# Kernel optimization log

Hardware: AMD Instinct MI355X
Metric: run time of the kernel (lower is better)

## Reference

```python
import jax, jax.numpy as jnp
import numpy as np

B, H, W = 8, 512, 512
N_INST = 8
N_SIGMA = 2
FG_W = 1.0
W_INST, W_VAR, W_SEED = 1.0, 10.0, 1.0


def make_yxm():
    xm = jnp.broadcast_to(jnp.linspace(0.0, 1.0, W)[None, None, :], (1, H, W))
    ym = jnp.broadcast_to(jnp.linspace(0.0, 1.0, H)[None, :, None], (1, H, W))
    return jnp.concatenate([ym, xm], 0)  # [2,H,W]


def lovasz_hinge(logits, labels):
    # logits, labels: [P]; labels in {0,1}
    signs = 2.0 * labels - 1.0
    errors = 1.0 - logits * signs
    order = jnp.argsort(-errors)
    errors_s = errors[order]
    gt_s = labels[order]
    gts = gt_s.sum()
    intersection = gts - jnp.cumsum(gt_s)
    union = gts + jnp.cumsum(1.0 - gt_s)
    jac = 1.0 - intersection / union
    jac = jnp.concatenate([jac[:1], jac[1:] - jac[:-1]])
    return jnp.dot(jax.nn.relu(errors_s), jax.lax.stop_gradient(jac))


def seg_item(pred, inst, label, center_img, yxm):
    spatial_emb = jnp.tanh(pred[0:2]) + yxm            # [2,H,W]
    sigma = jax.nn.sigmoid(pred[2:2 + N_SIGMA])        # [2,H,W]
    seed = jax.nn.sigmoid(pred[2 + N_SIGMA])           # [H,W]
    seed_loss = jnp.sum(jnp.where(label == 0, seed * seed, 0.0))

    def per_inst(iid):
        in_mask = (inst == iid)
        cmask = in_mask & center_img
        valid = (cmask.sum() == 1)                      # exactly one center pixel
        m = in_mask.astype(pred.dtype)
        npix = jnp.maximum(m.sum(), 1.0)
        center = jnp.sum(yxm * cmask, axis=(1, 2))      # [2]
        s_mean = jnp.sum(sigma * m, axis=(1, 2)) / npix # [2]
        var_l = jnp.sum(((sigma - jax.lax.stop_gradient(s_mean)[:, None, None]) ** 2) * m) / (N_SIGMA * npix)
        s = jnp.exp(s_mean * 10.0)
        dist = jnp.exp(-jnp.sum(((spatial_emb - center[:, None, None]) ** 2) * s[:, None, None], axis=0))
        inst_l = lovasz_hinge((dist * 2.0 - 1.0).ravel(), m.ravel())
        seed_l = jnp.sum(((seed - jax.lax.stop_gradient(dist)) ** 2) * m)
        v = valid.astype(pred.dtype)
        return inst_l * v, var_l * v, seed_l * v

    il, vl, sl = jax.vmap(per_inst)(jnp.arange(1, N_INST + 1))
    # NOTE: source never increments obj_count in the seg loop, so no division.
    seed_total = (seed_loss + FG_W * sl.sum()) / (H * W)
    return W_INST * il.sum() + W_VAR * vl.sum() + W_SEED * seed_total


def tra_item(pred, inst, center_img, offset, yxm):
    emb = yxm - jnp.tanh(pred[0:2])
    sigma = jax.nn.sigmoid(pred[2:2 + N_SIGMA])

    def per_inst(iid):
        in_mask = (inst == iid)
        cmask = in_mask & center_img
        center = jnp.sum(yxm * cmask, axis=(1, 2))          # [2]
        off_c = jnp.sum(offset * cmask, axis=(1, 2))        # [2]
        gt_c = center - off_c / 256.0
        valid = (cmask.sum() == 1) & (gt_c.min() >= 0.0) & (gt_c.max() <= 1.0)
        m = in_mask.astype(pred.dtype)
        npix = jnp.maximum(m.sum(), 1.0)
        s_mean = jnp.sum(sigma * m, axis=(1, 2)) / npix
        var_l = jnp.sum(((sigma - jax.lax.stop_gradient(s_mean)[:, None, None]) ** 2) * m)  # sum (not mean)
        s = jnp.exp(s_mean * 10.0)
        dist = jnp.exp(-jnp.sum(((emb - gt_c[:, None, None]) ** 2) * s[:, None, None], axis=0))
        tl = lovasz_hinge((dist * 2.0 - 1.0).ravel(), m.ravel())
        v = valid.astype(pred.dtype)
        return tl * v, var_l * v, v

    tl, vl, vs = jax.vmap(per_inst)(jnp.arange(1, N_INST + 1))
    cnt = jnp.maximum(vs.sum(), 1.0)
    return W_INST * (tl.sum() / cnt) + W_VAR * (vl.sum() / cnt)


def setup_inputs() -> dict:
    key = jax.random.key(0)
    k1, k2, k3 = jax.random.split(key, 3)
    inst = np.zeros((H, W), np.int32)
    cen = np.zeros((H, W), bool)
    for i in range(N_INST):
        ty, tx = i // 2, i % 2
        cy, cx = ty * 128 + 64, tx * 256 + 128
        inst[cy - 40:cy + 40, cx - 40:cx + 40] = i + 1
        cen[cy, cx] = True
    instances = jnp.tile(jnp.asarray(inst)[None], (B, 1, 1))
    center_images = jnp.tile(jnp.asarray(cen)[None], (B, 1, 1))
    labels = (instances > 0).astype(jnp.int32)
    return {
        "segmentation_predictions": jax.random.normal(k1, (B, 3 + N_SIGMA, H, W), jnp.float32),
        "tracking_predictions": jax.random.normal(k2, (B // 2, 2 + N_SIGMA, H, W), jnp.float32),
        "instances": instances,
        "labels": labels,
        "center_images": center_images,
        "offsets": jax.random.normal(k3, (B // 2, 2, H, W), jnp.float32),
    }


def reference(segmentation_predictions, tracking_predictions, instances, labels, center_images, offsets):
    yxm = make_yxm()
    seg = jax.vmap(seg_item, in_axes=(0, 0, 0, 0, None))(
        segmentation_predictions, instances, labels, center_images, yxm)
    half = B // 2
    tra = jax.vmap(tra_item, in_axes=(0, 0, 0, 0, None))(
        tracking_predictions, instances[:half], center_images[:half], offsets, yxm)
    return seg.sum() + tra.sum()
```

## Files before the change

kernel.cpp:

```cpp
#include <hip/hip_runtime.h>
#include <cstdint>
#include <cstddef>

#define HW (512 * 512)
#define NB3 512
#define NPAIR 96
#define THRQ 6.3f
#define BSCALE 256.0f

__device__ __forceinline__ float sigmoidf_(float x) {
    return 1.0f / (1.0f + __expf(-x));
}
__device__ __forceinline__ float tanhf_(float x) {
    float e = __expf(2.0f * x);
    return 1.0f - 2.0f / (e + 1.0f);
}
__device__ __forceinline__ float wred(float v) {
#pragma unroll
    for (int o = 32; o > 0; o >>= 1) v += __shfl_down(v, o, 64);
    return v;
}
__device__ __forceinline__ unsigned wredu(unsigned v) {
#pragma unroll
    for (int o = 32; o > 0; o >>= 1) v += __shfl_down(v, o, 64);
    return v;
}

__global__ __launch_bounds__(256) void zero_ws_k(unsigned* ws, int n) {
    int i = blockIdx.x * 256 + threadIdx.x;
    if (i < n) ws[i] = 0u;
}

__global__ __launch_bounds__(256) void reduce_k(
    const float* __restrict__ segp, const float* __restrict__ trap,
    const int* __restrict__ inst, const int* __restrict__ cen,
    const float* __restrict__ off,
    float* __restrict__ pacc, float* __restrict__ seedloss)
{
    __shared__ float part[4][41];
    int item = blockIdx.y;
    bool isseg = item < 8;
    int ii = isseg ? item : item - 8;
    const float* pb = isseg ? segp + (size_t)item * 5 * HW
                            : trap + (size_t)ii * 4 * HW;
    const int* ib = inst + (size_t)ii * HW;
    const int* cb = cen + (size_t)ii * HW;
    const float* ob = off + (size_t)ii * 2 * HW;
    int pairBase = (isseg ? 0 : 64) + ii * 8;

    float npx[8], a0[8], q0[8], a1[8], q1[8];
#pragma unroll
    for (int j = 0; j < 8; j++) { npx[j]=0.f; a0[j]=0.f; q0[j]=0.f; a1[j]=0.f; q1[j]=0.f; }
    float sacc = 0.f;

    int base = blockIdx.x * 4096;
    for (int it = 0; it < 4; ++it) {
        int idx = base + (it * 256 + threadIdx.x) * 4;
        int4 v4 = *(const int4*)&ib[idx];
        const int vs[4] = { v4.x, v4.y, v4.z, v4.w };
        if (isseg) {
            float4 x4 = *(const float4*)&pb[4 * HW + idx];
            const float ss[4] = { x4.x, x4.y, x4.z, x4.w };
#pragma unroll
            for (int c = 0; c < 4; c++) {
                if (vs[c] == 0) { float sd = sigmoidf_(ss[c]); sacc += sd * sd; }
            }
        }
        if ((v4.x | v4.y | v4.z | v4.w) != 0) {
            float4 x2 = *(const float4*)&pb[2 * HW + idx];
            float4 x3 = *(const float4*)&pb[3 * HW + idx];
            int4 c4 = *(const int4*)&cb[idx];
            const float s2s[4] = { x2.x, x2.y, x2.z, x2.w };
            const float s3s[4] = { x3.x, x3.y, x3.z, x3.w };
            const int cs[4] = { c4.x, c4.y, c4.z, c4.w };
#pragma unroll
            for (int c = 0; c < 4; c++) {
                int v = vs[c];
                if (v == 0) continue;
                float s0 = sigmoidf_(s2s[c]);
                float s1 = sigmoidf_(s3s[c]);
                float s00 = s0 * s0, s11 = s1 * s1;
#pragma unroll
                for (int j = 0; j < 8; j++) {
                    float f = (v == j + 1) ? 1.0f : 0.0f;
                    npx[j] += f;
                    a0[j] += f * s0; q0[j] += f * s00;
                    a1[j] += f * s1; q1[j] += f * s11;
                }
                if (cs[c] != 0 && v >= 1 && v <= 8) {
                    int idxc = idx + c;
                    int pair = pairBase + (v - 1);
                    int y = idxc >> 9, x = idxc & 511;
                    atomicAdd(&pacc[pair * 10 + 5], (float)y * (1.0f / 511.0f));
                    atomicAdd(&pacc[pair * 10 + 6], (float)x * (1.0f / 511.0f));
                    atomicAdd(&pacc[pair * 10 + 7], 1.0f);
                    if (!isseg) {
                        atomicAdd(&pacc[pair * 10 + 8], ob[idxc]);
                        atomicAdd(&pacc[pair * 10 + 9], ob[HW + idxc]);
                    }
                }
            }
        }
    }
    int lane = threadIdx.x & 63, wave = threadIdx.x >> 6;
#pragma unroll
    for (int j = 0; j < 8; j++) {
        float r0 = wred(npx[j]), r1 = wred(a0[j]), r2 = wred(q0[j]);
        float r3 = wred(a1[j]), r4 = wred(q1[j]);
        if (lane == 0) {
            part[wave][j * 5 + 0] = r0; part[wave][j * 5 + 1] = r1;
            part[wave][j * 5 + 2] = r2; part[wave][j * 5 + 3] = r3;
            part[wave][j * 5 + 4] = r4;
        }
    }
    {
        float rs = wred(sacc);
        if (lane == 0) part[wave][40] = rs;
    }
    __syncthreads();
    int t = threadIdx.x;
    if (t < 41) {
        float s = part[0][t] + part[1][t] + part[2][t] + part[3][t];
        if (t < 40) {
            int pair = pairBase + t / 5, comp = t % 5;
            atomicAdd(&pacc[pair * 10 + comp], s);
        } else if (isseg) {
            atomicAdd(&seedloss[item], s);
        }
    }
}

__global__ __launch_bounds__(256) void hist_k(
    const float* __restrict__ segp, const float* __restrict__ trap,
    const int* __restrict__ inst, const float* __restrict__ pacc,
    unsigned* __restrict__ hneg, unsigned* __restrict__ hpos,
    float* __restrict__ seedl)
{
    __shared__ unsigned hh[8 * NB3 + 8];
    __shared__ float prm[8][4];
    int item = blockIdx.y;
    bool isseg = item < 8;
    int ii = isseg ? item : item - 8;
    int tid = threadIdx.x;
    int pairBase = (isseg ? 0 : 64) + ii * 8;

    for (int i = tid; i < 8 * NB3 + 8; i += 256) hh[i] = 0u;
    if (tid < 8) {
        const float* a = pacc + (size_t)(pairBase + tid) * 10;
        float np = fmaxf(a[0], 1.0f);
        float cy = a[5], cx = a[6];
        if (!isseg) { cy -= a[8] * (1.0f / 256.0f); cx -= a[9] * (1.0f / 256.0f); }
        prm[tid][0] = cy;
        prm[tid][1] = cx;
        prm[tid][2] = __expf(10.0f * a[1] / np);
        prm[tid][3] = __expf(10.0f * a[3] / np);
    }
    __syncthreads();

    float cyR[8], cxR[8], s0R[8], s1R[8];
#pragma unroll
    for (int j = 0; j < 8; j++) {
        cyR[j] = prm[j][0]; cxR[j] = prm[j][1];
        s0R[j] = prm[j][2]; s1R[j] = prm[j][3];
    }
    const float* pb = isseg ? segp + (size_t)item * 5 * HW
                            : trap + (size_t)ii * 4 * HW;
    const int* ib = inst + (size_t)ii * HW;

    unsigned cnt0[8];
#pragma unroll
    for (int j = 0; j < 8; j++) cnt0[j] = 0u;

    int base = blockIdx.x * 2048;
    for (int it = 0; it < 4; ++it) {
        int idx = base + (it * 256 + tid) * 2;
        int2 v2 = *(const int2*)&ib[idx];
        float2 f0 = *(const float2*)&pb[idx];
        float2 f1 = *(const float2*)&pb[HW + idx];
        const int vv[2] = { v2.x, v2.y };
        const float p0s[2] = { f0.x, f0.y };
        const float p1s[2] = { f1.x, f1.y };
#pragma unroll
        for (int c = 0; c < 2; c++) {
            int idxc = idx + c;
            int v = vv[c];
            int y = idxc >> 9, x = idxc & 511;
            float ym = (float)y * (1.0f / 511.0f);
            float xm = (float)x * (1.0f / 511.0f);
            float t0 = tanhf_(p0s[c]), t1 = tanhf_(p1s[c]);
            float e0 = isseg ? (t0 + ym) : (ym - t0);
            float e1 = isseg ? (t1 + xm) : (xm - t1);
            unsigned sbits = 0u;
#pragma unroll
            for (int j = 0; j < 8; j++) {
                float d0 = e0 - cyR[j], d1 = e1 - cxR[j];
                float q = fmaf(d0 * d0, s0R[j], d1 * d1 * s1R[j]);
                bool m = (v == j + 1);
                bool slow = m || (q <= THRQ);
                sbits |= (slow ? 1u : 0u) << j;
                cnt0[j] += slow ? 0u : 1u;
            }
            while (sbits) {
                int j = __ffs(sbits) - 1;
                sbits &= sbits - 1u;
                float d0 = e0 - prm[j][0], d1 = e1 - prm[j][1];
                float q = fmaf(d0 * d0, prm[j][2], d1 * d1 * prm[j][3]);
                float dd = __expf(-q);
                bool m = (v == j + 1);
                float e = m ? fmaf(-2.0f, dd, 2.0f) : 2.0f * dd;
                int bin = (int)(e * BSCALE);
                if (bin > NB3 - 1) bin = NB3 - 1;
                atomicAdd(&hh[j * NB3 + bin], m ? 0x10000u : 1u);
                if (m && isseg) {
                    float sd = sigmoidf_(pb[4 * HW + idxc]);
                    float df = sd - dd;
                    atomicAdd((float*)&hh[8 * NB3 + j], df * df);
                }
            }
        }
    }
    int lane = tid & 63;
#pragma unroll
    for (int j = 0; j < 8; j++) {
        unsigned r = wredu(cnt0[j]);
        if (lane == 0 && r) atomicAdd(&hh[j * NB3], r);
    }
    __syncthreads();

#pragma unroll
    for (int j = 0; j < 8; j++) {
        size_t gb = (size_t)(pairBase + j) * NB3;
        for (int i = tid; i < NB3; i += 256) {
            unsigned hv = hh[j * NB3 + i];
            if (hv) {
                unsigned n = hv & 0xFFFFu, p = hv >> 16;
                if (n) atomicAdd(&hneg[gb + i], n);
                if (p) atomicAdd(&hpos[gb + i], p);
            }
        }
    }
    if (isseg && tid < 8) {
        float sv = __uint_as_float(hh[8 * NB3 + tid]);
        if (sv != 0.0f) atomicAdd(&seedl[pairBase + tid], sv);
    }
}

__global__ __launch_bounds__(64) void scan_k(
    const unsigned* __restrict__ hneg, const unsigned* __restrict__ hpos,
    float* __restrict__ lov)
{
    int pair = blockIdx.x;
    int lane = threadIdx.x;
    const unsigned* hn = hneg + (size_t)pair * NB3;
    const unsigned* hp = hpos + (size_t)pair * NB3;

    unsigned hnv[8], hpv[8];
    float ck = 0.f, cp = 0.f;
#pragma unroll
    for (int i = 0; i < 8; i++) {
        int bn = NB3 - 1 - (lane * 8 + i);
        unsigned a = hn[bn], b = hp[bn];
        hnv[i] = a; hpv[i] = b;
        ck += (float)(a + b); cp += (float)b;
    }
    float ik = ck, ip = cp;
#pragma unroll
    for (int o = 1; o < 64; o <<= 1) {
        float nk = __shfl_up(ik, o, 64), np2 = __shfl_up(ip, o, 64);
        if (lane >= o) { ik += nk; ip += np2; }
    }
    float P = __shfl(ip, 63, 64);
    float k = ik - ck;
    float p = ip - cp;
    float acc = 0.f;
#pragma unroll
    for (int i = 0; i < 8; i++) {
        float cn = (float)hnv[i], cpp = (float)hpv[i];
        float c = cn + cpp;
        if (c > 0.f) {
            float Jb = (k > 0.f) ? (1.0f - (P - p) / (P + k - p)) : 0.0f;
            k += c; p += cpp;
            float Ja = 1.0f - (P - p) / (P + k - p);
            int bn = NB3 - 1 - (lane * 8 + i);
            acc += ((float)bn + 0.5f) * (2.0f / NB3) * (Ja - Jb);
        }
    }
    acc = wred(acc);
    if (lane == 0) lov[pair] = acc;
}

__global__ __launch_bounds__(128) void combine_k(
    const float* __restrict__ pacc, const float* __restrict__ lov,
    const float* __restrict__ seedl, const float* __restrict__ seedloss,
    float* __restrict__ out)
{
    __shared__ float svalid[NPAIR], svar[NPAIR];
    int t = threadIdx.x;
    if (t < NPAIR) {
        const float* a = pacc + (size_t)t * 10;
        float npraw = a[0];
        float np = fmaxf(npraw, 1.0f);
        float v0 = fmaxf(a[2] - a[1] * a[1] / np, 0.0f);
        float v1 = fmaxf(a[4] - a[3] * a[3] / np, 0.0f);
        float cc = a[7];
        float valid, varl;
        if (t < 64) {
            varl = (v0 + v1) / (2.0f * np);
            valid = (cc > 0.5f && cc < 1.5f) ? 1.0f : 0.0f;
        } else {
            varl = v0 + v1;
            float gy = a[5] - a[8] * (1.0f / 256.0f);
            float gx = a[6] - a[9] * (1.0f / 256.0f);
            valid = (cc > 0.5f && cc < 1.5f &&
                     gy >= 0.0f && gy <= 1.0f && gx >= 0.0f && gx <= 1.0f) ? 1.0f : 0.0f;
        }
        svalid[t] = valid; svar[t] = varl;
    }
    __syncthreads();
    if (t == 0) {
        double total = 0.0;
        for (int b = 0; b < 8; b++) {
            double s = 0.0, sl = 0.0;
            for (int j = 0; j < 8; j++) {
                int pr = b * 8 + j;
                double v = svalid[pr];
                s += v * ((double)lov[pr] + 10.0 * (double)svar[pr]);
                sl += v * (double)seedl[pr];
            }
            total += s + ((double)seedloss[b] + sl) / (double)HW;
        }
        for (int tt = 0; tt < 4; tt++) {
            double tl = 0.0, vl = 0.0, cnt = 0.0;
            for (int j = 0; j < 8; j++) {
                int pr = 64 + tt * 8 + j;
                double v = svalid[pr];
                tl += v * (double)lov[pr];
                vl += v * (double)svar[pr];
                cnt += v;
            }
            if (cnt < 1.0) cnt = 1.0;
            total += tl / cnt + 10.0 * vl / cnt;
        }
        *out = (float)total;
    }
}

extern "C" void kernel_launch(void* const* d_in, const int* in_sizes, int n_in,
                              void* d_out, int out_size, void* d_ws, size_t ws_size,
                              hipStream_t stream)
{
    const float* segp = (const float*)d_in[0];
    const float* trap = (const float*)d_in[1];
    const int* inst   = (const int*)d_in[2];
    const int* cen    = (const int*)d_in[4];
    const float* off  = (const float*)d_in[5];
    float* out = (float*)d_out;

    unsigned* hneg = (unsigned*)d_ws;
    unsigned* hpos = hneg + (size_t)NPAIR * NB3;
    float* pacc = (float*)(hpos + (size_t)NPAIR * NB3);
    float* seedloss = pacc + NPAIR * 10;
    float* seedl = seedloss + 8;
    float* lov = seedl + NPAIR;
    size_t total_words = (size_t)NPAIR * NB3 * 2 + NPAIR * 10 + 8 + NPAIR + NPAIR;

    zero_ws_k<<<(int)((total_words + 255) / 256), 256, 0, stream>>>((unsigned*)d_ws, (int)total_words);
    reduce_k<<<dim3(64, 12), 256, 0, stream>>>(segp, trap, inst, cen, off, pacc, seedloss);
    hist_k<<<dim3(128, 12), 256, 0, stream>>>(segp, trap, inst, pacc, hneg, hpos, seedl);
    scan_k<<<NPAIR, 64, 0, stream>>>(hneg, hpos, lov);
    combine_k<<<1, 128, 0, stream>>>(pacc, lov, seedl, seedloss, out);
}
```

Baseline: 64.20 us.

## Merge zero and combine kernels, replace atomics with partial arrays, shrink histogram

Zeroing of the workspace moves into the reduce kernel. Global atomic accumulation is replaced by per-block partial arrays, which the histogram and scan kernels reduce themselves. The combine step is folded into the scan kernel behind a last-block counter, so the pipeline drops from five launches to three. The histogram shrinks from 512 to 128 bins with a lower cutoff threshold, and the histogram kernel now processes 4 pixels per thread over half as many blocks. The coarser bins and changed threshold alter how closely the Lovasz hinge is approximated, which risks accuracy.

Result: no change. 64.03 us (-0.3%).

```diff
diff --git a/kernel.cpp b/kernel.cpp
--- a/kernel.cpp
+++ b/kernel.cpp
@@ -3,10 +3,18 @@
 #include <cstddef>
 
 #define HW (512 * 512)
-#define NB3 512
+#define NB 128
 #define NPAIR 96
-#define THRQ 6.3f
-#define BSCALE 256.0f
+#define THRQ 4.9f
+#define BSCALE 64.0f
+
+#define W_HNEG 0
+#define W_HPOS (NPAIR * NB)
+#define W_SEEDL (NPAIR * NB * 2)
+#define W_CNT (W_SEEDL + NPAIR)
+#define NZERO (W_CNT + 1)
+#define W_PART 24704
+#define W_POUT (W_PART + 12 * 82 * 64)
 
 __device__ __forceinline__ float sigmoidf_(float x) {
     return 1.0f / (1.0f + __expf(-x));
@@ -26,36 +34,39 @@
     return v;
 }
 
-__global__ __launch_bounds__(256) void zero_ws_k(unsigned* ws, int n) {
-    int i = blockIdx.x * 256 + threadIdx.x;
-    if (i < n) ws[i] = 0u;
-}
-
-__global__ __launch_bounds__(256) void reduce_k(
+__global__ __launch_bounds__(256) void reduce_nc(
     const float* __restrict__ segp, const float* __restrict__ trap,
     const int* __restrict__ inst, const int* __restrict__ cen,
-    const float* __restrict__ off,
-    float* __restrict__ pacc, float* __restrict__ seedloss)
+    const float* __restrict__ off, float* __restrict__ ws)
 {
-    __shared__ float part[4][41];
+    __shared__ float wavepart[4][41];
+    __shared__ float centacc[40];
     int item = blockIdx.y;
     bool isseg = item < 8;
     int ii = isseg ? item : item - 8;
+    int bx = blockIdx.x, tid = threadIdx.x;
+
+    {
+        int w = (item * 64 + bx) * 33 + tid;
+        if (tid < 33 && w < NZERO) ws[w] = 0.0f;
+    }
+    if (tid < 40) centacc[tid] = 0.0f;
+    __syncthreads();
+
     const float* pb = isseg ? segp + (size_t)item * 5 * HW
                             : trap + (size_t)ii * 4 * HW;
     const int* ib = inst + (size_t)ii * HW;
     const int* cb = cen + (size_t)ii * HW;
     const float* ob = off + (size_t)ii * 2 * HW;
-    int pairBase = (isseg ? 0 : 64) + ii * 8;
 
     float npx[8], a0[8], q0[8], a1[8], q1[8];
 #pragma unroll
     for (int j = 0; j < 8; j++) { npx[j]=0.f; a0[j]=0.f; q0[j]=0.f; a1[j]=0.f; q1[j]=0.f; }
     float sacc = 0.f;
 
-    int base = blockIdx.x * 4096;
+    int base = bx * 4096;
     for (int it = 0; it < 4; ++it) {
-        int idx = base + (it * 256 + threadIdx.x) * 4;
+        int idx = base + (it * 256 + tid) * 4;
         int4 v4 = *(const int4*)&ib[idx];
         const int vs[4] = { v4.x, v4.y, v4.z, v4.w };
         if (isseg) {
@@ -89,54 +100,55 @@
                 }
                 if (cs[c] != 0 && v >= 1 && v <= 8) {
                     int idxc = idx + c;
-                    int pair = pairBase + (v - 1);
+                    int cb5 = (v - 1) * 5;
                     int y = idxc >> 9, x = idxc & 511;
-                    atomicAdd(&pacc[pair * 10 + 5], (float)y * (1.0f / 511.0f));
-                    atomicAdd(&pacc[pair * 10 + 6], (float)x * (1.0f / 511.0f));
-                    atomicAdd(&pacc[pair * 10 + 7], 1.0f);
+                    atomicAdd(&centacc[cb5 + 0], (float)y * (1.0f / 511.0f));
+                    atomicAdd(&centacc[cb5 + 1], (float)x * (1.0f / 511.0f));
+                    atomicAdd(&centacc[cb5 + 2], 1.0f);
                     if (!isseg) {
-                        atomicAdd(&pacc[pair * 10 + 8], ob[idxc]);
-                        atomicAdd(&pacc[pair * 10 + 9], ob[HW + idxc]);
+                        atomicAdd(&centacc[cb5 + 3], ob[idxc]);
+                        atomicAdd(&centacc[cb5 + 4], ob[HW + idxc]);
                     }
                 }
             }
         }
     }
-    int lane = threadIdx.x & 63, wave = threadIdx.x >> 6;
+    int lane = tid & 63, wave = tid >> 6;
 #pragma unroll
     for (int j = 0; j < 8; j++) {
         float r0 = wred(npx[j]), r1 = wred(a0[j]), r2 = wred(q0[j]);
         float r3 = wred(a1[j]), r4 = wred(q1[j]);
         if (lane == 0) {
-            part[wave][j * 5 + 0] = r0; part[wave][j * 5 + 1] = r1;
-            part[wave][j * 5 + 2] = r2; part[wave][j * 5 + 3] = r3;
-            part[wave][j * 5 + 4] = r4;
+            wavepart[wave][j * 5 + 0] = r0; wavepart[wave][j * 5 + 1] = r1;
+            wavepart[wave][j * 5 + 2] = r2; wavepart[wave][j * 5 + 3] = r3;
+            wavepart[wave][j * 5 + 4] = r4;
         }
     }
     {
         float rs = wred(sacc);
-        if (lane == 0) part[wave][40] = rs;
-    }
-    __syncthreads();
-    int t = threadIdx.x;
-    if (t < 41) {
-        float s = part[0][t] + part[1][t] + part[2][t] + part[3][t];
-        if (t < 40) {
-            int pair = pairBase + t / 5, comp = t % 5;
-            atomicAdd(&pacc[pair * 10 + comp], s);
-        } else if (isseg) {
-            atomicAdd(&seedloss[item], s);
-        }
+        if (lane == 0) wavepart[wave][40] = rs;
+    }
+    __syncthreads();
+    float* pit = ws + W_PART + item * 82 * 64;
+    if (tid < 40) {
+        pit[tid * 64 + bx] = wavepart[0][tid] + wavepart[1][tid] + wavepart[2][tid] + wavepart[3][tid];
+    } else if (tid == 40) {
+        pit[80 * 64 + bx] = wavepart[0][40] + wavepart[1][40] + wavepart[2][40] + wavepart[3][40];
+    } else if (tid >= 41 && tid < 81) {
+        pit[(40 + tid - 41) * 64 + bx] = centacc[tid - 41];
+    } else if (tid == 81) {
+        pit[81 * 64 + bx] = 0.0f;
     }
 }
 
 __global__ __launch_bounds__(256) void hist_k(
     const float* __restrict__ segp, const float* __restrict__ trap,
-    const int* __restrict__ inst, const float* __restrict__ pacc,
+    const int* __restrict__ inst, const float* __restrict__ ws,
     unsigned* __restrict__ hneg, unsigned* __restrict__ hpos,
     float* __restrict__ seedl)
 {
-    __shared__ unsigned hh[8 * NB3 + 8];
+    __shared__ unsigned hh[8 * NB + 8];
+    __shared__ float csum[82];
     __shared__ float prm[8][4];
     int item = blockIdx.y;
     bool isseg = item < 8;
@@ -144,16 +156,27 @@
     int tid = threadIdx.x;
     int pairBase = (isseg ? 0 : 64) + ii * 8;
 
-    for (int i = tid; i < 8 * NB3 + 8; i += 256) hh[i] = 0u;
+    for (int i = tid; i < 8 * NB + 8; i += 256) hh[i] = 0u;
+    if (tid < 82) {
+        const float* pit = ws + W_PART + item * 82 * 64 + tid * 64;
+        float s = 0.f;
+#pragma unroll 8
+        for (int b = 0; b < 64; b++) s += pit[b];
+        csum[tid] = s;
+    }
+    __syncthreads();
     if (tid < 8) {
-        const float* a = pacc + (size_t)(pairBase + tid) * 10;
-        float np = fmaxf(a[0], 1.0f);
-        float cy = a[5], cx = a[6];
-        if (!isseg) { cy -= a[8] * (1.0f / 256.0f); cx -= a[9] * (1.0f / 256.0f); }
-        prm[tid][0] = cy;
-        prm[tid][1] = cx;
-        prm[tid][2] = __expf(10.0f * a[1] / np);
-        prm[tid][3] = __expf(10.0f * a[3] / np);
+        int j = tid;
+        float np = fmaxf(csum[j * 5], 1.0f);
+        float cy = csum[40 + j * 5], cx = csum[40 + j * 5 + 1];
+        if (!isseg) {
+            cy -= csum[40 + j * 5 + 3] * (1.0f / 256.0f);
+            cx -= csum[40 + j * 5 + 4] * (1.0f / 256.0f);
+        }
+        prm[j][0] = cy;
+        prm[j][1] = cx;
+        prm[j][2] = __expf(10.0f * csum[j * 5 + 1] / np);
+        prm[j][3] = __expf(10.0f * csum[j * 5 + 3] / np);
     }
     __syncthreads();
 
@@ -171,17 +194,17 @@
 #pragma unroll
     for (int j = 0; j < 8; j++) cnt0[j] = 0u;
 
-    int base = blockIdx.x * 2048;
+    int base = blockIdx.x * 4096;
     for (int it = 0; it < 4; ++it) {
-        int idx = base + (it * 256 + tid) * 2;
-        int2 v2 = *(const int2*)&ib[idx];
-        float2 f0 = *(const float2*)&pb[idx];
-        float2 f1 = *(const float2*)&pb[HW + idx];
-        const int vv[2] = { v2.x, v2.y };
-        const float p0s[2] = { f0.x, f0.y };
-        const float p1s[2] = { f1.x, f1.y };
-#pragma unroll
-        for (int c = 0; c < 2; c++) {
+        int idx = base + (it * 256 + tid) * 4;
+        int4 v4 = *(const int4*)&ib[idx];
+        float4 f0 = *(const float4*)&pb[idx];
+        float4 f1 = *(const float4*)&pb[HW + idx];
+        const int vv[4] = { v4.x, v4.y, v4.z, v4.w };
+        const float p0s[4] = { f0.x, f0.y, f0.z, f0.w };
+        const float p1s[4] = { f1.x, f1.y, f1.z, f1.w };
+#pragma unroll
+        for (int c = 0; c < 4; c++) {
             int idxc = idx + c;
             int v = vv[c];
             int y = idxc >> 9, x = idxc & 511;
@@ -209,12 +232,12 @@
                 bool m = (v == j + 1);
                 float e = m ? fmaf(-2.0f, dd, 2.0f) : 2.0f * dd;
                 int bin = (int)(e * BSCALE);
-                if (bin > NB3 - 1) bin = NB3 - 1;
-                atomicAdd(&hh[j * NB3 + bin], m ? 0x10000u : 1u);
+                if (bin > NB - 1) bin = NB - 1;
+                atomicAdd(&hh[j * NB + bin], m ? 0x10000u : 1u);
                 if (m && isseg) {
                     float sd = sigmoidf_(pb[4 * HW + idxc]);
                     float df = sd - dd;
-                    atomicAdd((float*)&hh[8 * NB3 + j], df * df);
+                    atomicAdd((float*)&hh[8 * NB + j], df * df);
                 }
             }
         }
@@ -223,15 +246,18 @@
 #pragma unroll
     for (int j = 0; j < 8; j++) {
         unsigned r = wredu(cnt0[j]);
-        if (lane == 0 && r) atomicAdd(&hh[j * NB3], r);
+        if (lane == 0 && r) atomicAdd(&hh[j * NB], r);
     }
     __syncthreads();
 
 #pragma unroll
     for (int j = 0; j < 8; j++) {
-        size_t gb = (size_t)(pairBase + j) * NB3;
-        for (int i = tid; i < NB3; i += 256) {
-            unsigned hv = hh[j * NB3 + i];
+        size_t gb = (size_t)(pairBase + j) * NB;
+        for (int i = tid & 127; i < NB; i += 128) {
+            if ((tid >> 7) == 0 || 1) {}
+        }
+        for (int i = tid; i < NB; i += 256) {
+            unsigned hv = hh[j * NB + i];
             if (hv) {
                 unsigned n = hv & 0xFFFFu, p = hv >> 16;
                 if (n) atomicAdd(&hneg[gb + i], n);
@@ -240,25 +266,43 @@
         }
     }
     if (isseg && tid < 8) {
-        float sv = __uint_as_float(hh[8 * NB3 + tid]);
+        float sv = __uint_as_float(hh[8 * NB + tid]);
         if (sv != 0.0f) atomicAdd(&seedl[pairBase + tid], sv);
     }
 }
 
-__global__ __launch_bounds__(64) void scan_k(
-    const unsigned* __restrict__ hneg, const unsigned* __restrict__ hpos,
-    float* __restrict__ lov)
+__global__ __launch_bounds__(64) void scanfin_k(
+    float* __restrict__ ws, const unsigned* __restrict__ hneg,
+    const unsigned* __restrict__ hpos, const float* __restrict__ seedl,
+    unsigned* __restrict__ cntr, float* __restrict__ out)
 {
-    int pair = blockIdx.x;
+    __shared__ float fin[NPAIR * 4 + 8];
+    int p = blockIdx.x;
     int lane = threadIdx.x;
-    const unsigned* hn = hneg + (size_t)pair * NB3;
-    const unsigned* hp = hpos + (size_t)pair * NB3;
-
-    unsigned hnv[8], hpv[8];
+    int item12 = (p < 64) ? (p >> 3) : (8 + ((p - 64) >> 3));
+    int j = p & 7;
+    const float* pit = ws + W_PART + item12 * 82 * 64;
+
+    float r0 = pit[(j * 5 + 0) * 64 + lane];
+    float r1 = pit[(j * 5 + 1) * 64 + lane];
+    float r2 = pit[(j * 5 + 2) * 64 + lane];
+    float r3 = pit[(j * 5 + 3) * 64 + lane];
+    float r4 = pit[(j * 5 + 4) * 64 + lane];
+    float c0 = pit[(40 + j * 5 + 0) * 64 + lane];
+    float c1 = pit[(40 + j * 5 + 1) * 64 + lane];
+    float c2 = pit[(40 + j * 5 + 2) * 64 + lane];
+    float c3 = pit[(40 + j * 5 + 3) * 64 + lane];
+    float c4 = pit[(40 + j * 5 + 4) * 64 + lane];
+    r0 = wred(r0); r1 = wred(r1); r2 = wred(r2); r3 = wred(r3); r4 = wred(r4);
+    c0 = wred(c0); c1 = wred(c1); c2 = wred(c2); c3 = wred(c3); c4 = wred(c4);
+
+    const unsigned* hn = hneg + (size_t)p * NB;
+    const unsigned* hp = hpos + (size_t)p * NB;
+    unsigned hnv[2], hpv[2];
     float ck = 0.f, cp = 0.f;
 #pragma unroll
-    for (int i = 0; i < 8; i++) {
-        int bn = NB3 - 1 - (lane * 8 + i);
+    for (int i = 0; i < 2; i++) {
+        int bn = NB - 1 - (lane * 2 + i);
         unsigned a = hn[bn], b = hp[bn];
         hnv[i] = a; hpv[i] = b;
         ck += (float)(a + b); cp += (float)b;
@@ -270,72 +314,80 @@
         if (lane >= o) { ik += nk; ip += np2; }
     }
     float P = __shfl(ip, 63, 64);
-    float k = ik - ck;
-    float p = ip - cp;
+    float k = ik - ck, pp = ip - cp;
     float acc = 0.f;
 #pragma unroll
-    for (int i = 0; i < 8; i++) {
+    for (int i = 0; i < 2; i++) {
         float cn = (float)hnv[i], cpp = (float)hpv[i];
         float c = cn + cpp;
         if (c > 0.f) {
-            float Jb = (k > 0.f) ? (1.0f - (P - p) / (P + k - p)) : 0.0f;
-            k += c; p += cpp;
-            float Ja = 1.0f - (P - p) / (P + k - p);
-            int bn = NB3 - 1 - (lane * 8 + i);
-            acc += ((float)bn + 0.5f) * (2.0f / NB3) * (Ja - Jb);
+            float Jb = (k > 0.f) ? (1.0f - (P - pp) / (P + k - pp)) : 0.0f;
+            k += c; pp += cpp;
+            float Ja = 1.0f - (P - pp) / (P + k - pp);
+            int bn = NB - 1 - (lane * 2 + i);
+            acc += ((float)bn + 0.5f) * (2.0f / NB) * (Ja - Jb);
         }
     }
     acc = wred(acc);
-    if (lane == 0) lov[pair] = acc;
-}
-
-__global__ __launch_bounds__(128) void combine_k(
-    const float* __restrict__ pacc, const float* __restrict__ lov,
-    const float* __restrict__ seedl, const float* __restrict__ seedloss,
-    float* __restrict__ out)
-{
-    __shared__ float svalid[NPAIR], svar[NPAIR];
-    int t = threadIdx.x;
-    if (t < NPAIR) {
-        const float* a = pacc + (size_t)t * 10;
-        float npraw = a[0];
-        float np = fmaxf(npraw, 1.0f);
-        float v0 = fmaxf(a[2] - a[1] * a[1] / np, 0.0f);
-        float v1 = fmaxf(a[4] - a[3] * a[3] / np, 0.0f);
-        float cc = a[7];
+
+    if (lane == 0) {
+        float np = fmaxf(r0, 1.0f);
+        float v0 = fmaxf(r2 - r1 * r1 / np, 0.0f);
+        float v1 = fmaxf(r4 - r3 * r3 / np, 0.0f);
         float valid, varl;
-        if (t < 64) {
+        if (p < 64) {
             varl = (v0 + v1) / (2.0f * np);
-            valid = (cc > 0.5f && cc < 1.5f) ? 1.0f : 0.0f;
+            valid = (c2 > 0.5f && c2 < 1.5f) ? 1.0f : 0.0f;
         } else {
             varl = v0 + v1;
-            float gy = a[5] - a[8] * (1.0f / 256.0f);
-            float gx = a[6] - a[9] * (1.0f / 256.0f);
-            valid = (cc > 0.5f && cc < 1.5f &&
+            float gy = c0 - c3 * (1.0f / 256.0f);
+            float gx = c1 - c4 * (1.0f / 256.0f);
+            valid = (c2 > 0.5f && c2 < 1.5f &&
                      gy >= 0.0f && gy <= 1.0f && gx >= 0.0f && gx <= 1.0f) ? 1.0f : 0.0f;
         }
-        svalid[t] = valid; svar[t] = varl;
-    }
-    __syncthreads();
-    if (t == 0) {
+        float* po = ws + W_POUT + p * 4;
+        po[0] = acc; po[1] = valid; po[2] = varl; po[3] = 0.0f;
+    }
+    __threadfence();
+    unsigned old = 0;
+    if (lane == 0) old = atomicAdd(cntr, 1u);
+    old = (unsigned)__shfl((int)old, 0, 64);
+    if (old != NPAIR - 1) return;
+
+    __threadfence();
+    volatile float* pv = ws + W_POUT;
+    for (int q = lane; q < NPAIR; q += 64) {
+        fin[q * 4 + 0] = pv[q * 4 + 0];
+        fin[q * 4 + 1] = pv[q * 4 + 1];
+        fin[q * 4 + 2] = pv[q * 4 + 2];
+        fin[q * 4 + 3] = seedl[q];
+    }
+#pragma unroll
+    for (int b = 0; b < 8; b++) {
+        float s = ws[W_PART + b * 82 * 64 + 80 * 64 + lane];
+        s = wred(s);
+        if (lane == 0) fin[NPAIR * 4 + b] = s;
+    }
+    __syncthreads();
+    if (lane == 0) {
         double total = 0.0;
         for (int b = 0; b < 8; b++) {
             double s = 0.0, sl = 0.0;
-            for (int j = 0; j < 8; j++) {
-                int pr = b * 8 + j;
-                double v = svalid[pr];
-                s += v * ((double)lov[pr] + 10.0 * (double)svar[pr]);
-                sl += v * (double)seedl[pr];
-            }
-            total += s + ((double)seedloss[b] + sl) / (double)HW;
+            for (int jj = 0; jj < 8; jj++) {
+                int pr = b * 8 + jj;
+                double v = fin[pr * 4 + 1];
+                s += v * ((double)fin[pr * 4 + 0] + 10.0 * (double)fin[pr * 4 + 2]);
+                sl += v * (double)fin[pr * 4 + 3];
+            }
+            total += s + ((double)fin[NPAIR * 4 + b] + sl) / (double)HW;
         }
         for (int tt = 0; tt < 4; tt++) {
             double tl = 0.0, vl = 0.0, cnt = 0.0;
-            for (int j = 0; j < 8; j++) {
-                int pr = 64 + tt * 8 + j;
-                double v = svalid[pr];
-                tl += v * (double)lov[pr];
-                vl += v * (double)svar[pr];
+            for (int jj = 0; jj < 8; jj++) {
+                int pr = 64 + tt * 8 + jj;
+                double v = fin[pr * 4 + 1];
+                tl += v * (double)fin[pr * 4 + 0];
+                vl += v * (double)fin[pr * 4 + 2];
                 cnt += v;
             }
             if (cnt < 1.0) cnt = 1.0;
@@ -356,17 +408,13 @@
     const float* off  = (const float*)d_in[5];
     float* out = (float*)d_out;
 
-    unsigned* hneg = (unsigned*)d_ws;
-    unsigned* hpos = hneg + (size_t)NPAIR * NB3;
-    float* pacc = (float*)(hpos + (size_t)NPAIR * NB3);
-    float* seedloss = pacc + NPAIR * 10;
-    float* seedl = seedloss + 8;
-    float* lov = seedl + NPAIR;
-    size_t total_words = (size_t)NPAIR * NB3 * 2 + NPAIR * 10 + 8 + NPAIR + NPAIR;
-
-    zero_ws_k<<<(int)((total_words + 255) / 256), 256, 0, stream>>>((unsigned*)d_ws, (int)total_words);
-    reduce_k<<<dim3(64, 12), 256, 0, stream>>>(segp, trap, inst, cen, off, pacc, seedloss);
-    hist_k<<<dim3(128, 12), 256, 0, stream>>>(segp, trap, inst, pacc, hneg, hpos, seedl);
-    scan_k<<<NPAIR, 64, 0, stream>>>(hneg, hpos, lov);
-    combine_k<<<1, 128, 0, stream>>>(pacc, lov, seedl, seedloss, out);
-}
+    float* ws = (float*)d_ws;
+    unsigned* hneg = (unsigned*)d_ws + W_HNEG;
+    unsigned* hpos = (unsigned*)d_ws + W_HPOS;
+    float* seedl = ws + W_SEEDL;
+    unsigned* cntr = (unsigned*)d_ws + W_CNT;
+
+    reduce_nc<<<dim3(64, 12), 256, 0, stream>>>(segp, trap, inst, cen, off, ws);
+    hist_k<<<dim3(64, 12), 256, 0, stream>>>(segp, trap, inst, ws, hneg, hpos, seedl);
+    scanfin_k<<<NPAIR, 64, 0, stream>>>(ws, hneg, hpos, seedl, cntr, out);
+}
```
